# Performance work log

Measured on AMD Instinct MI355X. Metric: run time of the kernel, lower is better.

## Reference

```python
import jax, jax.numpy as jnp
import numpy as np

BOUNDING_PERC = 0.05

def setup_inputs() -> dict:
    key = jax.random.key(0)
    ks = jax.random.split(key, 8)
    b, nfaces, ncells, nb, in_dim, ksz = 4, 1_000_000, 500_000, 500_000, 4, 9
    kernel = jax.random.normal(ks[0], (b, nfaces, in_dim), dtype=jnp.float32)
    source = jax.random.normal(ks[1], (b, nfaces, 3, 3), dtype=jnp.float32)
    ucenters = jax.random.normal(ks[2], (b, ncells), dtype=jnp.float32)
    W = jax.random.normal(ks[3], (in_dim, ksz), dtype=jnp.float32)
    bias = jax.random.normal(ks[4], (ksz,), dtype=jnp.float32)
    positions = jnp.arange(nb, dtype=jnp.int32)  # unique boundary-face ids
    owners = jax.random.randint(ks[5], (nb,), 0, ncells, dtype=jnp.int32)
    neighbours = jax.random.randint(ks[6], (nb,), 0, ncells, dtype=jnp.int32)
    return {"kernel": kernel, "source": source, "ucenters": ucenters,
            "W": W, "bias": bias, "positions": positions,
            "owners": owners, "neighbours": neighbours}

def reference(kernel, source, ucenters, W, bias, positions, owners, neighbours):
    # constraint layer: affine map to per-face stencil coefficients [b, nfaces, ksz]
    coefficients = jnp.einsum('bxi,is->bxs', kernel, W) + bias
    b, nfaces = source.shape[0], source.shape[1]
    patches = source.reshape(b, nfaces, -1)          # [b, nfaces, ksz]
    ufaces = jnp.einsum('bxs,bxs->bx', coefficients, patches)  # [b, nfaces]
    # --- bounding on boundary faces ---
    ufaces_b = ufaces[:, positions]                   # [b, nb]
    owner = ucenters[:, owners]                       # [b, nb]
    neighbour = ucenters[:, neighbours]               # [b, nb]
    side_max = jnp.maximum(owner, neighbour)
    side_min = jnp.minimum(owner, neighbour)
    flux_cd = 0.5 * (owner + neighbour)
    upwind = jnp.where(flux_cd >= 0.0, owner, neighbour)
    upper_lim = side_max + BOUNDING_PERC * jnp.abs(side_max)
    lower_lim = side_min - BOUNDING_PERC * jnp.abs(side_min)
    valid = (ufaces_b >= lower_lim) & (ufaces_b <= upper_lim)
    ufaces_bounded = jnp.where(valid, ufaces_b, upwind)
    # scatter bounded values back into the full face array
    return ufaces.at[:, positions].set(ufaces_bounded)
```

## Files before the change

### kernel.cpp

```cpp
#include <hip/hip_runtime.h>

#define BOUNDING_PERC 0.05f

__global__ __launch_bounds__(256) void ufaces_kernel(
    const float4* __restrict__ k4,
    const float4* __restrict__ s4,
    const float*  __restrict__ W,
    const float*  __restrict__ bias,
    float4*       __restrict__ out,
    int nquads)
{
    int q = blockIdx.x * blockDim.x + threadIdx.x;
    if (q >= nquads) return;

    float Wr[4][9];
#pragma unroll
    for (int i = 0; i < 4; ++i)
#pragma unroll
        for (int s = 0; s < 9; ++s)
            Wr[i][s] = W[i * 9 + s];
    float br[9];
#pragma unroll
    for (int s = 0; s < 9; ++s) br[s] = bias[s];

    float4 kq[4];
#pragma unroll
    for (int f = 0; f < 4; ++f) kq[f] = k4[4 * q + f];

    float4 sv[9];
#pragma unroll
    for (int j = 0; j < 9; ++j) sv[j] = s4[9 * q + j];
    const float* S = reinterpret_cast<const float*>(sv);

    float4 res;
    float* rp = reinterpret_cast<float*>(&res);
#pragma unroll
    for (int f = 0; f < 4; ++f) {
        const float k0 = kq[f].x, k1 = kq[f].y, k2 = kq[f].z, k3 = kq[f].w;
        float acc = 0.0f;
#pragma unroll
        for (int s = 0; s < 9; ++s) {
            float c = br[s];
            c = fmaf(k0, Wr[0][s], c);
            c = fmaf(k1, Wr[1][s], c);
            c = fmaf(k2, Wr[2][s], c);
            c = fmaf(k3, Wr[3][s], c);
            acc = fmaf(c, S[9 * f + s], acc);
        }
        rp[f] = acc;
    }
    out[q] = res;
}

__global__ __launch_bounds__(256) void bound_kernel(
    const float* __restrict__ uc,
    const int*   __restrict__ pos,
    const int*   __restrict__ own,
    const int*   __restrict__ nei,
    float*       __restrict__ out,
    int nb, int nfaces, int ncells, int nbatch)
{
    int idx = blockIdx.x * blockDim.x + threadIdx.x;
    if (idx >= nbatch * nb) return;
    int j  = idx % nb;
    int bb = idx / nb;

    int p = pos[j];
    float uf = out[bb * nfaces + p];
    float o  = uc[bb * ncells + own[j]];
    float n  = uc[bb * ncells + nei[j]];

    float smax = fmaxf(o, n);
    float smin = fminf(o, n);
    float flux = 0.5f * (o + n);
    float up   = (flux >= 0.0f) ? o : n;
    float hi   = smax + BOUNDING_PERC * fabsf(smax);
    float lo   = smin - BOUNDING_PERC * fabsf(smin);
    bool valid = (uf >= lo) && (uf <= hi);
    out[bb * nfaces + p] = valid ? uf : up;
}

extern "C" void kernel_launch(void* const* d_in, const int* in_sizes, int n_in,
                              void* d_out, int out_size, void* d_ws, size_t ws_size,
                              hipStream_t stream)
{
    const float* kernel_in = (const float*)d_in[0];
    const float* source    = (const float*)d_in[1];
    const float* ucenters  = (const float*)d_in[2];
    const float* W         = (const float*)d_in[3];
    const float* bias      = (const float*)d_in[4];
    const int*   positions = (const int*)d_in[5];
    const int*   owners    = (const int*)d_in[6];
    const int*   neighbours= (const int*)d_in[7];
    float*       out       = (float*)d_out;

    const int b      = 4;
    const int in_dim = 4;
    const int nfaces = in_sizes[0] / (b * in_dim);
    const int ncells = in_sizes[2] / b;
    const int nb     = in_sizes[5];

    const int nquads = (b * nfaces) / 4;
    {
        dim3 block(256);
        dim3 grid((nquads + 255) / 256);
        ufaces_kernel<<<grid, block, 0, stream>>>(
            (const float4*)kernel_in, (const float4*)source, W, bias,
            (float4*)out, nquads);
    }

    {
        int total = b * nb;
        dim3 block(256);
        dim3 grid((total + 255) / 256);
        bound_kernel<<<grid, block, 0, stream>>>(
            ucenters, positions, owners, neighbours, out,
            nb, nfaces, ncells, b);
    }
}
```

Baseline: 63.62 us.

## Stage source patches through shared memory for coalesced loads, one face per thread

Each block now cooperatively loads its 256 faces' 9-float source patches into LDS with contiguous float4 loads, then each thread computes one face instead of four. This replaces the per-thread strided 36-float loads with fully coalesced block-wide loads and coalesced scalar stores. It adds a __syncthreads and LDS reads with a stride of 9 floats, and it drops the bounds check, so it assumes the face count is a multiple of 256.

```diff
diff --git a/kernel.cpp b/kernel.cpp
--- a/kernel.cpp
+++ b/kernel.cpp
@@ -7,11 +7,19 @@
     const float4* __restrict__ s4,
     const float*  __restrict__ W,
     const float*  __restrict__ bias,
-    float4*       __restrict__ out,
-    int nquads)
+    float*        __restrict__ out)
 {
-    int q = blockIdx.x * blockDim.x + threadIdx.x;
-    if (q >= nquads) return;
+    __shared__ float s_src[2304];
+    const int tid       = threadIdx.x;
+    const int base_face = blockIdx.x << 8;
+
+    {
+        const float4* src_blk = s4 + ((size_t)base_face * 9) / 4;
+        float4* sm4 = reinterpret_cast<float4*>(s_src);
+        sm4[tid]       = src_blk[tid];
+        sm4[tid + 256] = src_blk[tid + 256];
+        if (tid < 64) sm4[tid + 512] = src_blk[tid + 512];
+    }
 
     float Wr[4][9];
 #pragma unroll
@@ -23,33 +31,22 @@
 #pragma unroll
     for (int s = 0; s < 9; ++s) br[s] = bias[s];
 
-    float4 kq[4];
+    const float4 kv = k4[base_face + tid];
+
+    __syncthreads();
+
+    const float* S = &s_src[tid * 9];
+    float acc = 0.0f;
 #pragma unroll
-    for (int f = 0; f < 4; ++f) kq[f] = k4[4 * q + f];
-
-    float4 sv[9];
-#pragma unroll
-    for (int j = 0; j < 9; ++j) sv[j] = s4[9 * q + j];
-    const float* S = reinterpret_cast<const float*>(sv);
-
-    float4 res;
-    float* rp = reinterpret_cast<float*>(&res);
-#pragma unroll
-    for (int f = 0; f < 4; ++f) {
-        const float k0 = kq[f].x, k1 = kq[f].y, k2 = kq[f].z, k3 = kq[f].w;
-        float acc = 0.0f;
-#pragma unroll
-        for (int s = 0; s < 9; ++s) {
-            float c = br[s];
-            c = fmaf(k0, Wr[0][s], c);
-            c = fmaf(k1, Wr[1][s], c);
-            c = fmaf(k2, Wr[2][s], c);
-            c = fmaf(k3, Wr[3][s], c);
-            acc = fmaf(c, S[9 * f + s], acc);
-        }
-        rp[f] = acc;
+    for (int s = 0; s < 9; ++s) {
+        float c = br[s];
+        c = fmaf(kv.x, Wr[0][s], c);
+        c = fmaf(kv.y, Wr[1][s], c);
+        c = fmaf(kv.z, Wr[2][s], c);
+        c = fmaf(kv.w, Wr[3][s], c);
+        acc = fmaf(c, S[s], acc);
     }
-    out[q] = res;
+    out[base_face + tid] = acc;
 }
 
 __global__ __launch_bounds__(256) void bound_kernel(
@@ -84,15 +81,15 @@
                               void* d_out, int out_size, void* d_ws, size_t ws_size,
                               hipStream_t stream)
 {
-    const float* kernel_in = (const float*)d_in[0];
-    const float* source    = (const float*)d_in[1];
-    const float* ucenters  = (const float*)d_in[2];
-    const float* W         = (const float*)d_in[3];
-    const float* bias      = (const float*)d_in[4];
-    const int*   positions = (const int*)d_in[5];
-    const int*   owners    = (const int*)d_in[6];
-    const int*   neighbours= (const int*)d_in[7];
-    float*       out       = (float*)d_out;
+    const float* kernel_in  = (const float*)d_in[0];
+    const float* source     = (const float*)d_in[1];
+    const float* ucenters   = (const float*)d_in[2];
+    const float* W          = (const float*)d_in[3];
+    const float* bias       = (const float*)d_in[4];
+    const int*   positions  = (const int*)d_in[5];
+    const int*   owners     = (const int*)d_in[6];
+    const int*   neighbours = (const int*)d_in[7];
+    float*       out        = (float*)d_out;
 
     const int b      = 4;
     const int in_dim = 4;
@@ -100,13 +97,13 @@
     const int ncells = in_sizes[2] / b;
     const int nb     = in_sizes[5];
 
-    const int nquads = (b * nfaces) / 4;
+    const int total_faces = b * nfaces;
+
     {
         dim3 block(256);
-        dim3 grid((nquads + 255) / 256);
+        dim3 grid(total_faces / 256);
         ufaces_kernel<<<grid, block, 0, stream>>>(
-            (const float4*)kernel_in, (const float4*)source, W, bias,
-            (float4*)out, nquads);
+            (const float4*)kernel_in, (const float4*)source, W, bias, out);
     }
 
     {
```

New measurement: 60.82 us. 1.05x faster.
